# Kernel tuning notes

Hardware: AMD Instinct MI355X
Metric: run time of the kernel (lower is better)

The kernel has to match this reference:

```python
import jax, jax.numpy as jnp
import numpy as np
from jax import lax

DIM = 192
HEADS = 8
EPS = 1e-12  # F.normalize default eps


def conv(x, w, stride, pad, groups=1):
    return lax.conv_general_dilated(
        x, w, (stride, stride), [(pad, pad), (pad, pad)],
        dimension_numbers=('NCHW', 'OIHW', 'NCHW'),
        feature_group_count=groups)


def l2norm(t):
    # F.normalize(t, dim=-1): divide by max(||t||_2, eps)
    n = jnp.sqrt(jnp.sum(t * t, axis=-1, keepdims=True))
    return t / jnp.maximum(n, EPS)


def setup_inputs() -> dict:
    key = jax.random.key(0)
    ks = jax.random.split(key, 10)
    b, h, w = 4, 256, 256
    s = 0.05
    x = jax.random.normal(ks[0], (b, DIM, h, w), jnp.float32)
    illu_feat = jax.random.uniform(ks[1], (b, DIM, h, w), jnp.float32)
    wq = jax.random.normal(ks[2], (DIM, 1, 3, 3), jnp.float32) * s      # depthwise, groups=DIM
    wk = jax.random.normal(ks[3], (DIM, DIM, 3, 3), jnp.float32) * s
    wa_dw = jax.random.normal(ks[4], (DIM, 1, 3, 3), jnp.float32) * s   # depthwise
    wa_pw = jax.random.normal(ks[5], (DIM // 2, DIM, 1, 1), jnp.float32) * s
    ba_pw = jnp.zeros((DIM // 2,), jnp.float32)
    wv = jax.random.normal(ks[6], (DIM, DIM, 1, 1), jnp.float32) * s
    wo = jax.random.normal(ks[7], (DIM, DIM, 1, 1), jnp.float32) * s
    temp_a = jnp.ones((HEADS, 1, 1), jnp.float32)
    temp_v = jnp.ones((HEADS, 1, 1), jnp.float32)
    return dict(x=x, illu_feat=illu_feat, wq=wq, wk=wk, wa_dw=wa_dw,
                wa_pw=wa_pw, ba_pw=ba_pw, wv=wv, wo=wo,
                temp_a=temp_a, temp_v=temp_v)


def reference(x, illu_feat, wq, wk, wa_dw, wa_pw, ba_pw, wv, wo, temp_a, temp_v):
    b, c, h, w = x.shape
    q = conv(x, wq, 2, 1, groups=DIM)                 # [b, dim, h/2, w/2]
    k = conv(x, wk, 2, 1)                             # [b, dim, h/2, w/2]
    a = conv(conv(x, wa_dw, 2, 1, groups=DIM), wa_pw, 1, 0) + ba_pw[None, :, None, None]  # [b, dim/2, h/2, w/2]
    v = conv(x, wv, 1, 0) * illu_feat                 # [b, dim, h, w]

    def to_heads(t):
        bb, cc, hh, ww = t.shape
        return t.reshape(bb, HEADS, cc // HEADS, hh * ww)

    q, k, a, v = to_heads(q), to_heads(k), to_heads(a), to_heads(v)
    q, k, a = l2norm(q), l2norm(k), l2norm(a)

    # channel (transposed) attention: contract over spatial axis n
    attn_a = jnp.einsum('bhcn,bhdn->bhcd', q, a) * temp_a   # [b,H,c_q,c_a]
    attn_k = jnp.einsum('bhdn,bhcn->bhdc', a, k) * temp_v   # [b,H,c_a,c_k]
    out = jax.nn.softmax(attn_a, axis=-1) @ (jax.nn.softmax(attn_k, axis=-1) @ v)  # [b,H,c_q,h*w]
    out = out.reshape(b, c, h, w)
    return conv(out, wo, 1, 0)
```

## Files before the change

### kernel.cpp

```cpp
#include <hip/hip_runtime.h>
#include <stdint.h>

#define B 4
#define C 192
#define CA 96
#define HWN 65536
#define W2 128
#define HW2 16384
#define HEADS 8
#define CH 24
#define CAH 12

typedef short bf16x8 __attribute__((ext_vector_type(8)));
typedef short short4v __attribute__((ext_vector_type(4)));
typedef float f32x4 __attribute__((ext_vector_type(4)));
typedef unsigned int uint;

__device__ __forceinline__ float bf2f(short s) {
    union { uint u; float f; } v; v.u = ((uint)(unsigned short)s) << 16; return v.f;
}
__device__ __forceinline__ short f2bf(float f) {
    union { float f; uint u; } v; v.f = f;
    uint r = v.u + 0x7FFFu + ((v.u >> 16) & 1);
    return (short)(r >> 16);
}

__global__ __launch_bounds__(256) void k_pack(const float* wk, const float* wv, const float* wapw,
                                              short* wk_t, short* wv_b, short* wapw_b) {
    int i = blockIdx.x * 256 + threadIdx.x;
    if (i < 331776) {
        int tap = i / 36864, r = i % 36864;
        int co = r / C, ci = r % C;
        wk_t[i] = f2bf(wk[(co * C + ci) * 9 + tap]);
    } else if (i < 331776 + 36864) {
        int j = i - 331776;
        wv_b[j] = f2bf(wv[j]);
    } else if (i < 331776 + 36864 + 18432) {
        int j = i - 368640;
        wapw_b[j] = f2bf(wapw[j]);
    }
}

__global__ __launch_bounds__(256) void k_transpose(const float* x, short* xT) {
    int bid = blockIdx.x;
    int b = bid >> 10;
    int n0 = (bid & 1023) << 6;
    __shared__ float tile[64][193];
    const float* xb = x + (size_t)b * C * HWN;
    int t = threadIdx.x;
    for (int it = 0; it < 12; ++it) {
        int i = t + it * 256;
        int c = i >> 4;
        int j = i & 15;
        float4 v = *(const float4*)(xb + (size_t)c * HWN + n0 + j * 4);
        tile[j * 4 + 0][c] = v.x;
        tile[j * 4 + 1][c] = v.y;
        tile[j * 4 + 2][c] = v.z;
        tile[j * 4 + 3][c] = v.w;
    }
    __syncthreads();
    short* out = xT + ((size_t)b * HWN + n0) * C;
    for (int it = 0; it < 6; ++it) {
        int u = t + it * 256;
        int n = u / 24;
        int cp = u % 24;
        int c0 = cp * 8;
        bf16x8 vv;
#pragma unroll
        for (int k2 = 0; k2 < 8; ++k2) vv[k2] = f2bf(tile[n][c0 + k2]);
        *(bf16x8*)(out + (size_t)n * C + c0) = vv;
    }
}

__global__ __launch_bounds__(256) void k_kconv(const short* xT, const short* wk_t, short* kout) {
    int bid = blockIdx.x;
    int b = bid >> 8;
    int rem = bid & 255;
    int oh = rem >> 1;
    int owt = rem & 1;
    int tid = threadIdx.x;
    int lane = tid & 63;
    int wid = tid >> 6;
    int wm = wid & 1;
    int wn = wid >> 1;
    int l15 = lane & 15;
    int q = lane >> 4;

    f32x4 acc[6][2] = {};
    const short* xTb = xT + (size_t)b * HWN * C;
    int ow_base = owt * 64 + wn * 32;

    for (int tap = 0; tap < 9; ++tap) {
        int kh = tap / 3, kw = tap % 3;
        int ih = 2 * oh - 1 + kh;
        bool vrow = (unsigned)ih < 256u;
        int ihc = min(max(ih, 0), 255);
        const short* bp[2];
        bool bv[2];
#pragma unroll
        for (int nt = 0; nt < 2; ++nt) {
            int ow = ow_base + nt * 16 + l15;
            int iw = 2 * ow - 1 + kw;
            bv[nt] = vrow && ((unsigned)iw < 256u);
            int iwc = min(max(iw, 0), 255);
            bp[nt] = xTb + ((size_t)ihc * 256 + iwc) * C + q * 8;
        }
        const short* ap = wk_t + ((size_t)tap * C + (wm * 96 + l15)) * C + q * 8;
#pragma unroll
        for (int ks = 0; ks < 6; ++ks) {
            bf16x8 zf = {};
            bf16x8 bf[2];
#pragma unroll
            for (int nt = 0; nt < 2; ++nt) {
                bf16x8 raw = *(const bf16x8*)(bp[nt] + ks * 32);
                bf[nt] = bv[nt] ? raw : zf;
            }
#pragma unroll
            for (int mt = 0; mt < 6; ++mt) {
                bf16x8 af = *(const bf16x8*)(ap + (size_t)mt * 16 * C + ks * 32);
#pragma unroll
                for (int nt = 0; nt < 2; ++nt)
                    acc[mt][nt] = __builtin_amdgcn_mfma_f32_16x16x32_bf16(af, bf[nt], acc[mt][nt], 0, 0, 0);
            }
        }
    }
    __shared__ short lt[C][72];
#pragma unroll
    for (int mt = 0; mt < 6; ++mt)
#pragma unroll
        for (int nt = 0; nt < 2; ++nt) {
            int px = wn * 32 + nt * 16 + l15;
#pragma unroll
            for (int r = 0; r < 4; ++r) {
                int co = wm * 96 + mt * 16 + q * 4 + r;
                lt[co][px] = f2bf(acc[mt][nt][r]);
            }
        }
    __syncthreads();
    short* kb = kout + (size_t)b * C * HW2 + oh * W2 + owt * 64;
    for (int it = 0; it < 6; ++it) {
        int u = tid + it * 256;
        int co = u >> 3;
        int ch = u & 7;
        bf16x8 vv = *(const bf16x8*)(&lt[co][ch * 8]);
        *(bf16x8*)(kb + (size_t)co * HW2 + ch * 8) = vv;
    }
}

__global__ __launch_bounds__(256) void k_dw(const float* x, const float* wq, const float* wadw,
                                            short* qout, short* adwT) {
    int bid = blockIdx.x;
    int oh = bid & 127;
    int r2 = bid >> 7;
    int cg = r2 % 12;
    int b  = r2 / 12;
    int t = threadIdx.x;
    int og = t & 15;
    int cl = t >> 4;
    int c = cg * 16 + cl;
    int ow0 = og * 8;

    float wq_r[9], wa_r[9];
#pragma unroll
    for (int k9 = 0; k9 < 9; ++k9) { wq_r[k9] = wq[c * 9 + k9]; wa_r[k9] = wadw[c * 9 + k9]; }

    const float* xp = x + (size_t)(b * C + c) * HWN;
    float qa[8] = {}, aa[8] = {};
    int ibase = 2 * ow0 - 4;
#pragma unroll
    for (int kh = 0; kh < 3; ++kh) {
        int ih = 2 * oh - 1 + kh;
        if ((unsigned)ih >= 256u) continue;
        const float* rp = xp + (size_t)ih * 256;
        float arr[20];
#pragma unroll
        for (int ck = 0; ck < 5; ++ck) {
            int iw = ibase + ck * 4;
            if (iw >= 0) {
                float4 v = *(const float4*)(rp + iw);
                arr[ck * 4 + 0] = v.x; arr[ck * 4 + 1] = v.y;
                arr[ck * 4 + 2] = v.z; arr[ck * 4 + 3] = v.w;
            } else {
                arr[ck * 4 + 0] = 0.f; arr[ck * 4 + 1] = 0.f;
                arr[ck * 4 + 2] = 0.f; arr[ck * 4 + 3] = 0.f;
            }
        }
        float q0 = wq_r[kh * 3 + 0], q1 = wq_r[kh * 3 + 1], q2 = wq_r[kh * 3 + 2];
        float a0 = wa_r[kh * 3 + 0], a1 = wa_r[kh * 3 + 1], a2 = wa_r[kh * 3 + 2];
#pragma unroll
        for (int oz = 0; oz < 8; ++oz) {
            float s0 = arr[2 * oz + 3], s1 = arr[2 * oz + 4], s2 = arr[2 * oz + 5];
            qa[oz] += q0 * s0 + q1 * s1 + q2 * s2;
            aa[oz] += a0 * s0 + a1 * s1 + a2 * s2;
        }
    }

    bf16x8 qv;
#pragma unroll
    for (int oz = 0; oz < 8; ++oz) qv[oz] = f2bf(qa[oz]);
    *(bf16x8*)(qout + (size_t)(b * C + c) * HW2 + oh * W2 + ow0) = qv;

    __shared__ short la[128][17];
#pragma unroll
    for (int oz = 0; oz < 8; ++oz) la[ow0 + oz][cl] = f2bf(aa[oz]);
    __syncthreads();
    {
        int ow = t >> 1;
        int jh = (t & 1) * 8;
        bf16x8 vv;
#pragma unroll
        for (int j = 0; j < 8; ++j) vv[j] = la[ow][jh + j];
        short* dst = adwT + ((size_t)b * HW2 + (size_t)oh * W2 + ow) * C + cg * 16 + jh;
        *(bf16x8*)dst = vv;
    }
}

__global__ __launch_bounds__(256) void k_apw(const short* adwT, const short* wapw_b, const float* bapw,
                                             short* aout) {
    int bid = blockIdx.x;
    int b = bid >> 7;
    int op0 = (bid & 127) << 7;
    int tid = threadIdx.x;
    int lane = tid & 63;
    int wid = tid >> 6;
    int wm = wid & 1, wn = wid >> 1;
    int l15 = lane & 15, q = lane >> 4;
    f32x4 acc[3][4] = {};
    const short* bb = adwT + ((size_t)b * HW2 + op0 + wn * 64 + l15) * C + q * 8;
    const short* ab0 = wapw_b + (size_t)(wm * 48 + l15) * C + q * 8;
#pragma unroll
    for (int ks = 0; ks < 6; ++ks) {
        bf16x8 bf[4];
#pragma unroll
        for (int nt = 0; nt < 4; ++nt)
            bf[nt] = *(const bf16x8*)(bb + (size_t)nt * 16 * C + ks * 32);
#pragma unroll
        for (int mt = 0; mt < 3; ++mt) {
            bf16x8 af = *(const bf16x8*)(ab0 + (size_t)mt * 16 * C + ks * 32);
#pragma unroll
            for (int nt = 0; nt < 4; ++nt)
                acc[mt][nt] = __builtin_amdgcn_mfma_f32_16x16x32_bf16(af, bf[nt], acc[mt][nt], 0, 0, 0);
        }
    }
    __shared__ short la[CA][136];
#pragma unroll
    for (int mt = 0; mt < 3; ++mt)
#pragma unroll
        for (int nt = 0; nt < 4; ++nt) {
            int px = wn * 64 + nt * 16 + l15;
#pragma unroll
            for (int r = 0; r < 4; ++r) {
                int d = wm * 48 + mt * 16 + q * 4 + r;
                la[d][px] = f2bf(acc[mt][nt][r] + bapw[d]);
            }
        }
    __syncthreads();
    short* abp = aout + (size_t)b * CA * HW2 + op0;
    for (int it = 0; it < 6; ++it) {
        int u = tid + it * 256;
        int d = u >> 4;
        int ch = u & 15;
        bf16x8 vv = *(const bf16x8*)(&la[d][ch * 8]);
        *(bf16x8*)(abp + (size_t)d * HW2 + ch * 8) = vv;
    }
}

__global__ __launch_bounds__(64) void k_attn(const short* qb, const short* kb, const short* abuf,
                                             float* attn_a, float* attn_k,
                                             float* ssq, float* ssk, float* ssa) {
    int bid = blockIdx.x;
    int b = bid >> 9;
    int rem = bid & 511;
    int h = rem >> 6;
    int cid = rem & 63;
    int lane = threadIdx.x;
    int l15 = lane & 15, q = lane >> 4;
    int n_base = cid * 256 + q * 8;
    int c1 = min(16 + l15, 23);
    int da = min(l15, 11);
    const short* qrow0 = qb + ((size_t)(b * C + h * CH + l15)) * HW2 + n_base;
    const short* qrow1 = qb + ((size_t)(b * C + h * CH + c1)) * HW2 + n_base;
    const short* krow0 = kb + ((size_t)(b * C + h * CH + l15)) * HW2 + n_base;
    const short* krow1 = kb + ((size_t)(b * C + h * CH + c1)) * HW2 + n_base;
    const short* arow = abuf + ((size_t)(b * CA + h * CAH + da)) * HW2 + n_base;
    f32x4 aa[2] = {};
    f32x4 ak[2] = {};
    float sq0 = 0, sq1 = 0, sk0 = 0, sk1 = 0, sa0 = 0;
#pragma unroll
    for (int ks = 0; ks < 8; ++ks) {
        bf16x8 qf0 = *(const bf16x8*)(qrow0 + ks * 32);
        bf16x8 qf1 = *(const bf16x8*)(qrow1 + ks * 32);
        bf16x8 kf0 = *(const bf16x8*)(krow0 + ks * 32);
        bf16x8 kf1 = *(const bf16x8*)(krow1 + ks * 32);
        bf16x8 af = *(const bf16x8*)(arow + ks * 32);
        aa[0] = __builtin_amdgcn_mfma_f32_16x16x32_bf16(qf0, af, aa[0], 0, 0, 0);
        aa[1] = __builtin_amdgcn_mfma_f32_16x16x32_bf16(qf1, af, aa[1], 0, 0, 0);
        ak[0] = __builtin_amdgcn_mfma_f32_16x16x32_bf16(af, kf0, ak[0], 0, 0, 0);
        ak[1] = __builtin_amdgcn_mfma_f32_16x16x32_bf16(af, kf1, ak[1], 0, 0, 0);
#pragma unroll
        for (int j = 0; j < 8; ++j) {
            float f;
            f = bf2f(qf0[j]); sq0 += f * f;
            f = bf2f(qf1[j]); sq1 += f * f;
            f = bf2f(kf0[j]); sk0 += f * f;
            f = bf2f(kf1[j]); sk1 += f * f;
            f = bf2f(af[j]);  sa0 += f * f;
        }
    }
    sq0 += __shfl_xor(sq0, 16); sq0 += __shfl_xor(sq0, 32);
    sq1 += __shfl_xor(sq1, 16); sq1 += __shfl_xor(sq1, 32);
    sk0 += __shfl_xor(sk0, 16); sk0 += __shfl_xor(sk0, 32);
    sk1 += __shfl_xor(sk1, 16); sk1 += __shfl_xor(sk1, 32);
    sa0 += __shfl_xor(sa0, 16); sa0 += __shfl_xor(sa0, 32);
    if (lane < 16) atomicAdd(&ssq[b * C + h * CH + lane], sq0);
    if (lane < 8)  atomicAdd(&ssq[b * C + h * CH + 16 + lane], sq1);
    if (lane < 16) atomicAdd(&ssk[b * C + h * CH + lane], sk0);
    if (lane < 8)  atomicAdd(&ssk[b * C + h * CH + 16 + lane], sk1);
    if (lane < 12) atomicAdd(&ssa[b * CA + h * CAH + lane], sa0);

    float* pa = attn_a + (size_t)(b * HEADS + h) * CH * CAH;
#pragma unroll
    for (int mt = 0; mt < 2; ++mt)
#pragma unroll
        for (int r = 0; r < 4; ++r) {
            int cc = mt * 16 + q * 4 + r;
            if (cc < 24 && l15 < 12) atomicAdd(&pa[cc * CAH + l15], aa[mt][r]);
        }
    float* pk = attn_k + (size_t)(b * HEADS + h) * CAH * CH;
#pragma unroll
    for (int nt = 0; nt < 2; ++nt)
#pragma unroll
        for (int r = 0; r < 4; ++r) {
            int dd = q * 4 + r;
            int cc = nt * 16 + l15;
            if (dd < 12 && cc < 24) atomicAdd(&pk[dd * CH + cc], ak[nt][r]);
        }
}

__global__ __launch_bounds__(256) void k_soft(const float* ssq, const float* ssk, const float* ssa,
                                              const float* attn_a, const float* attn_k,
                                              const float* temp_a, const float* temp_v, float* Wout) {
    int b = blockIdx.x;
    int t = threadIdx.x;
    __shared__ float sq[C], sk[C], sa[CA];
    __shared__ float P[HEADS * CH * CAH];
    __shared__ float M[HEADS * CAH * CH];
    if (t < C) {
        sq[t] = 1.f / fmaxf(sqrtf(ssq[b * C + t]), 1e-12f);
        sk[t] = 1.f / fmaxf(sqrtf(ssk[b * C + t]), 1e-12f);
    }
    if (t < CA) sa[t] = 1.f / fmaxf(sqrtf(ssa[b * CA + t]), 1e-12f);
    __syncthreads();
    if (t < HEADS * CH) {
        int h = t / CH, c = t % CH;
        const float* src = attn_a + ((size_t)(b * HEADS + h) * CH + c) * CAH;
        float ta = temp_a[h];
        float row[CAH];
        float mx = -1e30f;
#pragma unroll
        for (int d = 0; d < CAH; ++d) {
            row[d] = src[d] * sq[h * CH + c] * sa[h * CAH + d] * ta;
            mx = fmaxf(mx, row[d]);
        }
        float s = 0;
#pragma unroll
        for (int d = 0; d < CAH; ++d) { row[d] = __expf(row[d] - mx); s += row[d]; }
        float inv = 1.f / s;
#pragma unroll
        for (int d = 0; d < CAH; ++d) P[(h * CH + c) * CAH + d] = row[d] * inv;
    }
    if (t < HEADS * CAH) {
        int h = t / CAH, d = t % CAH;
        const float* src = attn_k + ((size_t)(b * HEADS + h) * CAH + d) * CH;
        float tv = temp_v[h];
        float row[CH];
        float mx = -1e30f;
#pragma unroll
        for (int c = 0; c < CH; ++c) {
            row[c] = src[c] * sa[h * CAH + d] * sk[h * CH + c] * tv;
            mx = fmaxf(mx, row[c]);
        }
        float s = 0;
#pragma unroll
        for (int c = 0; c < CH; ++c) { row[c] = __expf(row[c] - mx); s += row[c]; }
        float inv = 1.f / s;
#pragma unroll
        for (int c = 0; c < CH; ++c) M[(h * CAH + d) * CH + c] = row[c] * inv;
    }
    __syncthreads();
    for (int i = t; i < HEADS * CH * CH; i += 256) {
        int h = i / (CH * CH);
        int rr = i % (CH * CH);
        int c = rr / CH, c2 = rr % CH;
        float s = 0;
#pragma unroll
        for (int d = 0; d < CAH; ++d) s += P[(h * CH + c) * CAH + d] * M[(h * CAH + d) * CH + c2];
        Wout[(size_t)b * HEADS * CH * CH + i] = s;
    }
}

__global__ __launch_bounds__(256) void k_buildU(const float* Wout, const float* wo, short* U_b) {
    int bid = blockIdx.x;
    int b = bid / 12;
    int co0 = (bid % 12) * 16;
    int t = threadIdx.x;
    __shared__ float Wl[HEADS * CH * CH];
    for (int i = t; i < HEADS * CH * CH; i += 256) Wl[i] = Wout[(size_t)b * HEADS * CH * CH + i];
    __syncthreads();
    for (int u = t; u < 16 * C; u += 256) {
        int col = u / C;
        int ci = u % C;
        int co = co0 + col;
        int h = ci / CH, c2 = ci % CH;
        float s = 0;
#pragma unroll
        for (int c = 0; c < CH; ++c) s += wo[(size_t)co * C + h * CH + c] * Wl[(h * CH + c) * CH + c2];
        U_b[((size_t)b * C + co) * C + ci] = f2bf(s);
    }
}

__global__ __launch_bounds__(256) void k_vout(const short* xT, const short* wv_b, const short* U_b,
                                              const float* illu, float* out) {
    int bid = blockIdx.x;
    int b = bid >> 10;
    int n0 = (bid & 1023) << 6;
    int tid = threadIdx.x;
    int lane = tid & 63;
    int wid = tid >> 6;
    int wm = wid & 1, wn = wid >> 1;
    int l15 = lane & 15, q = lane >> 4;
    __shared__ __align__(16) char lds_raw[C * 68 * 4];
    short* ldsT = (short*)lds_raw;
    float* ldsO = (float*)lds_raw;

    f32x4 acc1[6][2] = {};
    {
        const short* bb = xT + ((size_t)b * HWN + n0 + wn * 32 + l15) * C + q * 8;
        const short* ab = wv_b + (size_t)(wm * 96 + l15) * C + q * 8;
#pragma unroll
        for (int ks = 0; ks < 6; ++ks) {
            bf16x8 bf0 = *(const bf16x8*)(bb + ks * 32);
            bf16x8 bf1 = *(const bf16x8*)(bb + (size_t)16 * C + ks * 32);
#pragma unroll
            for (int mt = 0; mt < 6; ++mt) {
                bf16x8 af = *(const bf16x8*)(ab + (size_t)mt * 16 * C + ks * 32);
                acc1[mt][0] = __builtin_amdgcn_mfma_f32_16x16x32_bf16(af, bf0, acc1[mt][0], 0, 0, 0);
                acc1[mt][1] = __builtin_amdgcn_mfma_f32_16x16x32_bf16(af, bf1, acc1[mt][1], 0, 0, 0);
            }
        }
    }
    const float* ilb = illu + (size_t)b * C * HWN + n0;
#pragma unroll
    for (int mt = 0; mt < 6; ++mt)
#pragma unroll
        for (int nt = 0; nt < 2; ++nt) {
            int px = wn * 32 + nt * 16 + l15;
            short4v sv;
#pragma unroll
            for (int r = 0; r < 4; ++r) {
                int co = wm * 96 + mt * 16 + q * 4 + r;
                float il = ilb[(size_t)co * HWN + px];
                sv[r] = f2bf(acc1[mt][nt][r] * il);
            }
            *(short4v*)(&ldsT[px * 200 + wm * 96 + mt * 16 + q * 4]) = sv;
        }
    __syncthreads();
    f32x4 acc2[6][2] = {};
    {
        const short* ub = U_b + ((size_t)b * C + wm * 96 + l15) * C + q * 8;
        const short* tb = ldsT + (wn * 32 + l15) * 200 + q * 8;
#pragma unroll
        for (int ks = 0; ks < 6; ++ks) {
            bf16x8 bf0 = *(const bf16x8*)(tb + ks * 32);
            bf16x8 bf1 = *(const bf16x8*)(tb + 16 * 200 + ks * 32);
#pragma unroll
            for (int mt = 0; mt < 6; ++mt) {
                bf16x8 af = *(const bf16x8*)(ub + (size_t)mt * 16 * C + ks * 32);
                acc2[mt][0] = __builtin_amdgcn_mfma_f32_16x16x32_bf16(af, bf0, acc2[mt][0], 0, 0, 0);
                acc2[mt][1] = __builtin_amdgcn_mfma_f32_16x16x32_bf16(af, bf1, acc2[mt][1], 0, 0, 0);
            }
        }
    }
    __syncthreads();
#pragma unroll
    for (int mt = 0; mt < 6; ++mt)
#pragma unroll
        for (int nt = 0; nt < 2; ++nt) {
            int px = wn * 32 + nt * 16 + l15;
#pragma unroll
            for (int r = 0; r < 4; ++r) {
                int co = wm * 96 + mt * 16 + q * 4 + r;
                ldsO[co * 68 + px] = acc2[mt][nt][r];
            }
        }
    __syncthreads();
    float* ob = out + (size_t)b * C * HWN + n0;
    for (int it = 0; it < 12; ++it) {
        int u = tid + it * 256;
        int co = u >> 4;
        int ch = u & 15;
        float4 vv = *(const float4*)(&ldsO[co * 68 + ch * 4]);
        *(float4*)(ob + (size_t)co * HWN + ch * 4) = vv;
    }
}

extern "C" void kernel_launch(void* const* d_in, const int* in_sizes, int n_in,
                              void* d_out, int out_size, void* d_ws, size_t ws_size,
                              hipStream_t stream) {
    (void)in_sizes; (void)n_in; (void)out_size;
    const float* x      = (const float*)d_in[0];
    const float* illu   = (const float*)d_in[1];
    const float* wq     = (const float*)d_in[2];
    const float* wk     = (const float*)d_in[3];
    const float* wa_dw  = (const float*)d_in[4];
    const float* wa_pw  = (const float*)d_in[5];
    const float* ba_pw  = (const float*)d_in[6];
    const float* wv     = (const float*)d_in[7];
    const float* wo     = (const float*)d_in[8];
    const float* temp_a = (const float*)d_in[9];
    const float* temp_v = (const float*)d_in[10];
    float* out = (float*)d_out;

    char* ws = (char*)d_ws;
    size_t off = 0;
    auto alloc = [&](size_t bytes) -> void* {
        void* p = ws + off;
        off += (bytes + 255) & ~(size_t)255;
        return p;
    };
    short* xT     = (short*)alloc((size_t)B * HWN * C * 2);
    short* kbuf   = (short*)alloc((size_t)B * C * HW2 * 2);
    short* qbuf   = (short*)alloc((size_t)B * C * HW2 * 2);
    short* adwT   = (short*)alloc((size_t)B * HW2 * C * 2);
    short* abuf   = (short*)alloc((size_t)B * CA * HW2 * 2);
    short* wk_t   = (short*)alloc((size_t)9 * C * C * 2);
    short* wv_b   = (short*)alloc((size_t)C * C * 2);
    short* wapw_b = (short*)alloc((size_t)CA * C * 2);
    short* U_b    = (short*)alloc((size_t)B * C * C * 2);
    float* W_ws   = (float*)alloc((size_t)B * HEADS * CH * CH * 4);
    size_t accum_floats = (size_t)2 * B * C + B * CA + (size_t)2 * B * HEADS * CH * CAH;
    float* accum  = (float*)alloc(accum_floats * 4);
    float* ssq = accum;
    float* ssk = ssq + B * C;
    float* ssa = ssk + B * C;
    float* attn_a = ssa + B * CA;
    float* attn_k = attn_a + B * HEADS * CH * CAH;
    (void)ws_size;

    hipMemsetAsync(accum, 0, accum_floats * 4, stream);
    k_pack<<<1512, 256, 0, stream>>>(wk, wv, wa_pw, wk_t, wv_b, wapw_b);
    k_transpose<<<B * 1024, 256, 0, stream>>>(x, xT);
    k_kconv<<<1024, 256, 0, stream>>>(xT, wk_t, kbuf);
    k_dw<<<B * 12 * 128, 256, 0, stream>>>(x, wq, wa_dw, qbuf, adwT);
    k_apw<<<512, 256, 0, stream>>>(adwT, wapw_b, ba_pw, abuf);
    k_attn<<<2048, 64, 0, stream>>>(qbuf, kbuf, abuf, attn_a, attn_k, ssq, ssk, ssa);
    k_soft<<<B, 256, 0, stream>>>(ssq, ssk, ssa, attn_a, attn_k, temp_a, temp_v, W_ws);
    k_buildU<<<B * 12, 256, 0, stream>>>(W_ws, wo, U_b);
    k_vout<<<B * 1024, 256, 0, stream>>>(xT, wv_b, U_b, illu, out);
}
```

Baseline: 938.3 us.

## Double-buffer k-conv input taps in LDS via async global_load_lds and prefetch weights

The dense 3x3 stride-2 conv kernel now stages each tap's input pixels into a double-buffered LDS tile using direct global-to-LDS loads, reading from a zero buffer for padding. The next tap is loaded while MFMAs run on the current one. Weight fragments are register-prefetched one k-step ahead, and block IDs are remapped so concurrently running blocks share the same batch image. The goal is to hide global-load latency and cut redundant uncoalesced global reads, at the cost of more LDS and more registers, which may lower occupancy.

```diff
diff --git a/kernel.cpp b/kernel.cpp
--- a/kernel.cpp
+++ b/kernel.cpp
@@ -72,8 +72,10 @@
     }
 }
 
-__global__ __launch_bounds__(256) void k_kconv(const short* xT, const short* wk_t, short* kout) {
-    int bid = blockIdx.x;
+__global__ __launch_bounds__(256) void k_kconv(const short* xT, const short* wk_t, short* kout,
+                                               const short* zbuf) {
+    int orig = blockIdx.x;
+    int bid = (orig & 7) * 128 + (orig >> 3);
     int b = bid >> 8;
     int rem = bid & 255;
     int oh = rem >> 1;
@@ -86,45 +88,67 @@
     int l15 = lane & 15;
     int q = lane >> 4;
 
-    f32x4 acc[6][2] = {};
+    __shared__ __align__(16) short lB[2][12288];
+
     const short* xTb = xT + (size_t)b * HWN * C;
-    int ow_base = owt * 64 + wn * 32;
-
-    for (int tap = 0; tap < 9; ++tap) {
+    int px_s = tid & 63;
+    int gb = tid >> 6;
+    int ow_s = owt * 64 + px_s;
+
+    auto stage = [&](int tap, int nb) {
         int kh = tap / 3, kw = tap % 3;
         int ih = 2 * oh - 1 + kh;
-        bool vrow = (unsigned)ih < 256u;
-        int ihc = min(max(ih, 0), 255);
-        const short* bp[2];
-        bool bv[2];
-#pragma unroll
-        for (int nt = 0; nt < 2; ++nt) {
-            int ow = ow_base + nt * 16 + l15;
-            int iw = 2 * ow - 1 + kw;
-            bv[nt] = vrow && ((unsigned)iw < 256u);
-            int iwc = min(max(iw, 0), 255);
-            bp[nt] = xTb + ((size_t)ihc * 256 + iwc) * C + q * 8;
-        }
-        const short* ap = wk_t + ((size_t)tap * C + (wm * 96 + l15)) * C + q * 8;
+        int iw = 2 * ow_s - 1 + kw;
+        bool v = ((unsigned)ih < 256u) && ((unsigned)iw < 256u);
+        const short* src0 = v ? (xTb + ((size_t)ih * 256 + iw) * C) : zbuf;
+        short* db = &lB[nb][0] + tid * 8;
+#pragma unroll
+        for (int s = 0; s < 6; ++s) {
+            const short* sp = v ? (src0 + (gb + s * 4) * 8) : zbuf;
+            __builtin_amdgcn_global_load_lds(
+                (const __attribute__((address_space(1))) void*)sp,
+                (__attribute__((address_space(3))) void*)(db + s * 2048), 16, 0, 0);
+        }
+    };
+
+    f32x4 acc[6][2] = {};
+    bf16x8 afc[6], afn[6];
+    const short* ap = wk_t + (size_t)(wm * 96 + l15) * C + q * 8;
+
+    stage(0, 0);
+#pragma unroll
+    for (int mt = 0; mt < 6; ++mt) afc[mt] = *(const bf16x8*)(ap + (size_t)mt * 16 * C);
+    __syncthreads();
+
+    for (int tap = 0; tap < 9; ++tap) {
+        if (tap < 8) stage(tap + 1, (tap + 1) & 1);
+        const short* lbB = &lB[tap & 1][0];
 #pragma unroll
         for (int ks = 0; ks < 6; ++ks) {
-            bf16x8 zf = {};
-            bf16x8 bf[2];
-#pragma unroll
-            for (int nt = 0; nt < 2; ++nt) {
-                bf16x8 raw = *(const bf16x8*)(bp[nt] + ks * 32);
-                bf[nt] = bv[nt] ? raw : zf;
-            }
+            const short* apn = ap;
+            int ksn = ks + 1;
+            if (ks == 5) {
+                ksn = (tap < 8) ? 0 : 5;
+                apn = (tap < 8) ? (ap + C * C) : ap;
+            }
+#pragma unroll
+            for (int mt = 0; mt < 6; ++mt)
+                afn[mt] = *(const bf16x8*)(apn + (size_t)mt * 16 * C + ksn * 32);
+            bf16x8 bf0 = *(const bf16x8*)(lbB + ((ks * 4 + q) * 64 + wn * 32 + l15) * 8);
+            bf16x8 bf1 = *(const bf16x8*)(lbB + ((ks * 4 + q) * 64 + wn * 32 + 16 + l15) * 8);
 #pragma unroll
             for (int mt = 0; mt < 6; ++mt) {
-                bf16x8 af = *(const bf16x8*)(ap + (size_t)mt * 16 * C + ks * 32);
-#pragma unroll
-                for (int nt = 0; nt < 2; ++nt)
-                    acc[mt][nt] = __builtin_amdgcn_mfma_f32_16x16x32_bf16(af, bf[nt], acc[mt][nt], 0, 0, 0);
-            }
-        }
-    }
-    __shared__ short lt[C][72];
+                acc[mt][0] = __builtin_amdgcn_mfma_f32_16x16x32_bf16(afc[mt], bf0, acc[mt][0], 0, 0, 0);
+                acc[mt][1] = __builtin_amdgcn_mfma_f32_16x16x32_bf16(afc[mt], bf1, acc[mt][1], 0, 0, 0);
+            }
+#pragma unroll
+            for (int mt = 0; mt < 6; ++mt) afc[mt] = afn[mt];
+        }
+        ap += C * C;
+        __syncthreads();
+    }
+
+    short (*lt)[72] = (short (*)[72])(&lB[0][0]);
 #pragma unroll
     for (int mt = 0; mt < 6; ++mt)
 #pragma unroll
@@ -538,6 +562,7 @@
     short* wapw_b = (short*)alloc((size_t)CA * C * 2);
     short* U_b    = (short*)alloc((size_t)B * C * C * 2);
     float* W_ws   = (float*)alloc((size_t)B * HEADS * CH * CH * 4);
+    short* zbuf   = (short*)alloc(256);
     size_t accum_floats = (size_t)2 * B * C + B * CA + (size_t)2 * B * HEADS * CH * CAH;
     float* accum  = (float*)alloc(accum_floats * 4);
     float* ssq = accum;
@@ -548,9 +573,10 @@
     (void)ws_size;
 
     hipMemsetAsync(accum, 0, accum_floats * 4, stream);
+    hipMemsetAsync(zbuf, 0, 256, stream);
     k_pack<<<1512, 256, 0, stream>>>(wk, wv, wa_pw, wk_t, wv_b, wapw_b);
     k_transpose<<<B * 1024, 256, 0, stream>>>(x, xT);
-    k_kconv<<<1024, 256, 0, stream>>>(xT, wk_t, kbuf);
+    k_kconv<<<1024, 256, 0, stream>>>(xT, wk_t, kbuf, zbuf);
     k_dw<<<B * 12 * 128, 256, 0, stream>>>(x, wq, wa_dw, qbuf, adwT);
     k_apw<<<512, 256, 0, stream>>>(adwT, wapw_b, ba_pw, abuf);
     k_attn<<<2048, 64, 0, stream>>>(qbuf, kbuf, abuf, attn_a, attn_k, ssq, ssk, ssa);
```

Measured after the change: 911.9 us. 2.8% less time.
